# Performance work log

Measured on AMD Instinct MI355X. Metric: run time of the kernel, lower is better.

Reference implementation:

```python
import jax, jax.numpy as jnp
import numpy as np

NUM_CAPSULE = 16
DIM_CAPSULE = 64
ROUTINGS = 3
T_EPS = 1e-7


def setup_inputs() -> dict:
    key = jax.random.key(0)
    k1, k2 = jax.random.split(key)
    x = jax.random.normal(k1, (64, 512, 768), dtype=jnp.float32)
    # xavier-normal-ish init for W: [1, input_dim_capsule, num_capsule*dim_capsule]
    fan_in, fan_out = 768, NUM_CAPSULE * DIM_CAPSULE
    std = float(np.sqrt(2.0 / (fan_in + fan_out)))
    W = jax.random.normal(k2, (1, 768, NUM_CAPSULE * DIM_CAPSULE), dtype=jnp.float32) * std
    return {"x": x, "W": W}


def _squash(v, eps=T_EPS):
    # NOTE: this module's 'squash' is pure L2 normalization with eps, not the
    # classic (s^2/(1+s^2)) squash.
    s2 = jnp.sum(v * v, axis=-1, keepdims=True)
    return v / jnp.sqrt(s2 + eps)


def reference(x, W):
    B, In, _ = x.shape
    # u_hat: [B, In, num*dim] -> [B, num, In, dim]
    u = jnp.matmul(x, W).reshape(B, In, NUM_CAPSULE, DIM_CAPSULE).transpose(0, 2, 1, 3)
    b = jnp.zeros((B, NUM_CAPSULE, In), dtype=u.dtype)  # routing logits
    outputs = None
    for i in range(ROUTINGS):
        # torch code softmaxes over the num_capsule axis (after permute dance)
        c = jax.nn.softmax(b, axis=1)  # [B, num, In]
        outputs = _squash(jnp.einsum('bij,bijk->bik', c, u))  # [B, num, dim]
        if i < ROUTINGS - 1:
            b = jnp.einsum('bik,bijk->bij', outputs, u)  # [B, num, In]
    return outputs
```

## Files before the change

kernel.cpp:

```cpp
#include <hip/hip_runtime.h>
#include <hip/hip_bf16.h>
#include <stdint.h>

#define BATCH 64
#define IN_CAPS 512
#define NCAP 16
#define DCAP 64
#define GN (NCAP * DCAP)
#define GM (BATCH * IN_CAPS)
#define GK 768

typedef __bf16 bf16;
typedef __attribute__((ext_vector_type(8))) __bf16 bf16x8;
typedef __attribute__((ext_vector_type(4))) float f32x4;

__device__ inline void async16(const bf16* g, bf16* l) {
    __builtin_amdgcn_global_load_lds(
        (__attribute__((address_space(1))) void*)g,
        (__attribute__((address_space(3))) void*)l, 16, 0, 0);
}

__global__ __launch_bounds__(256) void k_convX2(const float* __restrict__ X,
                                                bf16* __restrict__ Xb,
                                                float* __restrict__ XS) {
    __shared__ float ls[GK];
    const int tid = threadIdx.x;
    ls[tid] = 0.f; ls[tid + 256] = 0.f; ls[tid + 512] = 0.f;
    __syncthreads();
    const size_t base = (size_t)blockIdx.x * (32 * GK);
    float acc[3][8] = {};
#pragma unroll
    for (int r = 0; r < 12; ++r) {
        const int off = r * 2048 + tid * 8;
        const f32x4 a0 = *(const f32x4*)(X + base + off);
        const f32x4 a1 = *(const f32x4*)(X + base + off + 4);
        bf16x8 o;
        o[0] = (bf16)a0[0]; o[1] = (bf16)a0[1]; o[2] = (bf16)a0[2]; o[3] = (bf16)a0[3];
        o[4] = (bf16)a1[0]; o[5] = (bf16)a1[1]; o[6] = (bf16)a1[2]; o[7] = (bf16)a1[3];
        *(bf16x8*)(Xb + base + off) = o;
        const int g = r % 3;
        acc[g][0] += a0[0]; acc[g][1] += a0[1];
        acc[g][2] += a0[2]; acc[g][3] += a0[3];
        acc[g][4] += a1[0]; acc[g][5] += a1[1];
        acc[g][6] += a1[2]; acc[g][7] += a1[3];
    }
    if (XS != nullptr) {
#pragma unroll
        for (int g = 0; g < 3; ++g) {
            const int cg = (g == 1) ? 512 : (g == 2) ? 256 : 0;
            const int kb = (tid * 8 + cg) % GK;
#pragma unroll
            for (int j = 0; j < 8; ++j) atomicAdd(&ls[kb + j], acc[g][j]);
        }
        __syncthreads();
        const int bidx = blockIdx.x >> 4;
        atomicAdd(&XS[(size_t)bidx * GK + tid],       ls[tid]);
        atomicAdd(&XS[(size_t)bidx * GK + tid + 256], ls[tid + 256]);
        atomicAdd(&XS[(size_t)bidx * GK + tid + 512], ls[tid + 512]);
    }
}

__global__ void k_transW(const float* __restrict__ W, bf16* __restrict__ Wt,
                         float* __restrict__ XS) {
    __shared__ bf16 t[32][33];
    const int k0 = blockIdx.x * 32;
    const int n0 = blockIdx.y * 32;
    const int tx = threadIdx.x, ty = threadIdx.y;
    if (XS != nullptr) {
        const int gid = (blockIdx.y * gridDim.x + blockIdx.x) * 256 + ty * 32 + tx;
        if (gid < BATCH * GK) XS[gid] = 0.f;
    }
#pragma unroll
    for (int r = 0; r < 4; ++r)
        t[ty + r * 8][tx] = (bf16)W[(size_t)(k0 + ty + r * 8) * GN + n0 + tx];
    __syncthreads();
#pragma unroll
    for (int r = 0; r < 4; ++r)
        Wt[(size_t)(n0 + ty + r * 8) * GK + k0 + tx] = t[tx][ty + r * 8];
}

__global__ __launch_bounds__(256) void k_out1(const float* __restrict__ XS,
                                              const float* __restrict__ W,
                                              float* __restrict__ O1) {
    __shared__ float xs[4][GK];
    __shared__ float red[4][4][64];
    const int cap = blockIdx.x & 15;
    const int bg = blockIdx.x >> 4;
    const int tid = threadIdx.x;
    const int k = tid & 63, kq = tid >> 6;
#pragma unroll
    for (int bb = 0; bb < 4; ++bb) {
        const size_t b = (size_t)(bg * 4 + bb);
        xs[bb][tid]       = XS[b * GK + tid];
        xs[bb][tid + 256] = XS[b * GK + tid + 256];
        xs[bb][tid + 512] = XS[b * GK + tid + 512];
    }
    __syncthreads();
    float acc4[4] = {0.f, 0.f, 0.f, 0.f};
    const float* wp = W + (size_t)(kq * 192) * GN + cap * 64 + k;
#pragma unroll 4
    for (int kk = 0; kk < 192; ++kk) {
        const float w = wp[(size_t)kk * GN];
        const int kx = kq * 192 + kk;
        acc4[0] += xs[0][kx] * w;
        acc4[1] += xs[1][kx] * w;
        acc4[2] += xs[2][kx] * w;
        acc4[3] += xs[3][kx] * w;
    }
#pragma unroll
    for (int bb = 0; bb < 4; ++bb) red[bb][kq][k] = acc4[bb];
    __syncthreads();
    if (tid < 64) {
#pragma unroll
        for (int bb = 0; bb < 4; ++bb) {
            float s = (red[bb][0][tid] + red[bb][1][tid] +
                       red[bb][2][tid] + red[bb][3][tid]) * 0.0625f;
            float ss = s * s;
#pragma unroll
            for (int off = 32; off >= 1; off >>= 1) ss += __shfl_xor(ss, off);
            O1[((size_t)(bg * 4 + bb) * NCAP + cap) * DCAP + tid] =
                s * rsqrtf(ss + 1e-7f);
        }
    }
}

__global__ __launch_bounds__(256) void k_gemm_async(const bf16* __restrict__ Xb,
                                                    const bf16* __restrict__ Wt,
                                                    const float* __restrict__ O1,
                                                    bf16* __restrict__ U,
                                                    float* __restrict__ BL) {
    __shared__ bf16 sA[128 * 32];
    __shared__ bf16 sB[128 * 32];

    const int tid = threadIdx.x;
    const int lane = tid & 63;
    const int wave = tid >> 6;
    const int wm = wave >> 1, wn = wave & 1;
    const int bid = blockIdx.x;
    const int swz = (bid & 7) * 256 + (bid >> 3);
    const int m0 = (swz >> 3) * 128;
    const int n0 = (swz & 7) * 128;

    const int c0 = wave * 2, c1 = wave * 2 + 1;
    const int rl = lane >> 2, cl = (lane & 3) * 8;
    const bf16* gA0 = Xb + (size_t)(m0 + c0 * 16 + rl) * GK + cl;
    const bf16* gA1 = Xb + (size_t)(m0 + c1 * 16 + rl) * GK + cl;
    const bf16* gB0 = Wt + (size_t)(n0 + c0 * 16 + rl) * GK + cl;
    const bf16* gB1 = Wt + (size_t)(n0 + c1 * 16 + rl) * GK + cl;
    bf16* lA0 = sA + c0 * 512;
    bf16* lA1 = sA + c1 * 512;
    bf16* lB0 = sB + c0 * 512;
    bf16* lB1 = sB + c1 * 512;

    f32x4 acc[4][4] = {};
    const int fr = lane & 15;
    const int fq = lane >> 4;

    for (int kt = 0; kt < GK / 32; ++kt) {
        __syncthreads();
        async16(gA0, lA0);
        async16(gA1, lA1);
        async16(gB0, lB0);
        async16(gB1, lB1);
        gA0 += 32; gA1 += 32; gB0 += 32; gB1 += 32;
        __syncthreads();

        bf16x8 af[4], bfr[4];
#pragma unroll
        for (int mi = 0; mi < 4; ++mi)
            af[mi] = *(const bf16x8*)(sA + (wm * 64 + mi * 16 + fr) * 32 + fq * 8);
#pragma unroll
        for (int ni = 0; ni < 4; ++ni)
            bfr[ni] = *(const bf16x8*)(sB + (wn * 64 + ni * 16 + fr) * 32 + fq * 8);
#pragma unroll
        for (int mi = 0; mi < 4; ++mi)
#pragma unroll
            for (int ni = 0; ni < 4; ++ni)
                acc[mi][ni] = __builtin_amdgcn_mfma_f32_16x16x32_bf16(
                    af[mi], bfr[ni], acc[mi][ni], 0, 0, 0);
    }

#pragma unroll
    for (int mi = 0; mi < 4; ++mi) {
#pragma unroll
        for (int ni = 0; ni < 4; ++ni) {
#pragma unroll
            for (int r = 0; r < 4; ++r) {
                const int m = m0 + wm * 64 + mi * 16 + fq * 4 + r;
                const int n = n0 + wn * 64 + ni * 16 + fr;
                const int bb = m >> 9, j = m & 511;
                const int ci = n >> 6, k = n & 63;
                U[(((size_t)(bb * NCAP + ci)) * IN_CAPS + j) * DCAP + k] =
                    (bf16)acc[mi][ni][r];
            }
        }
    }

    if (O1 != nullptr) {
        const int b = m0 >> 9;
        const int cap = (n0 >> 6) + wn;
        float o1v[4];
#pragma unroll
        for (int ni = 0; ni < 4; ++ni)
            o1v[ni] = O1[(size_t)b * GN + n0 + wn * 64 + ni * 16 + fr];
#pragma unroll
        for (int mi = 0; mi < 4; ++mi) {
#pragma unroll
            for (int r = 0; r < 4; ++r) {
                float p = o1v[0] * acc[mi][0][r] + o1v[1] * acc[mi][1][r] +
                          o1v[2] * acc[mi][2][r] + o1v[3] * acc[mi][3][r];
                p += __shfl_xor(p, 1);
                p += __shfl_xor(p, 2);
                p += __shfl_xor(p, 4);
                p += __shfl_xor(p, 8);
                if (fr == 0) {
                    const int j = (m0 & 511) + wm * 64 + mi * 16 + fq * 4 + r;
                    BL[((size_t)(b * NCAP + cap)) * IN_CAPS + j] = p;
                }
            }
        }
    }
}

__global__ __launch_bounds__(256) void k_gemm_inline(const float* __restrict__ X,
                                                     const bf16* __restrict__ Wt,
                                                     bf16* __restrict__ U) {
    __shared__ bf16 sA[128 * 32];
    __shared__ bf16 sB[128 * 32];
    const int tid = threadIdx.x;
    const int lane = tid & 63;
    const int wave = tid >> 6;
    const int wm = wave >> 1, wn = wave & 1;
    const int m0 = blockIdx.x * 128;
    const int n0 = blockIdx.y * 128;
    const int srow = tid >> 2;
    const int scol = (tid & 3) * 8;
    f32x4 acc[4][4] = {};
    const int fr = lane & 15;
    const int fq = lane >> 4;
    for (int kt = 0; kt < GK / 32; ++kt) {
        const int kb = kt * 32;
        bf16x8 a0, a1, b0, b1;
        {
            const float* p = X + (size_t)(m0 + srow) * GK + kb + scol;
            const f32x4 x0 = *(const f32x4*)p, x1 = *(const f32x4*)(p + 4);
            const float* q = X + (size_t)(m0 + srow + 64) * GK + kb + scol;
            const f32x4 y0 = *(const f32x4*)q, y1 = *(const f32x4*)(q + 4);
#pragma unroll
            for (int c = 0; c < 4; ++c) {
                a0[c] = (bf16)x0[c]; a0[c + 4] = (bf16)x1[c];
                a1[c] = (bf16)y0[c]; a1[c + 4] = (bf16)y1[c];
            }
        }
        b0 = *(const bf16x8*)(Wt + (size_t)(n0 + srow) * GK + kb + scol);
        b1 = *(const bf16x8*)(Wt + (size_t)(n0 + srow + 64) * GK + kb + scol);
        __syncthreads();
        *(bf16x8*)(sA + srow * 32 + scol) = a0;
        *(bf16x8*)(sA + (srow + 64) * 32 + scol) = a1;
        *(bf16x8*)(sB + srow * 32 + scol) = b0;
        *(bf16x8*)(sB + (srow + 64) * 32 + scol) = b1;
        __syncthreads();
        bf16x8 af[4], bfr[4];
#pragma unroll
        for (int mi = 0; mi < 4; ++mi)
            af[mi] = *(const bf16x8*)(sA + (wm * 64 + mi * 16 + fr) * 32 + fq * 8);
#pragma unroll
        for (int ni = 0; ni < 4; ++ni)
            bfr[ni] = *(const bf16x8*)(sB + (wn * 64 + ni * 16 + fr) * 32 + fq * 8);
#pragma unroll
        for (int mi = 0; mi < 4; ++mi)
#pragma unroll
            for (int ni = 0; ni < 4; ++ni)
                acc[mi][ni] = __builtin_amdgcn_mfma_f32_16x16x32_bf16(
                    af[mi], bfr[ni], acc[mi][ni], 0, 0, 0);
    }
#pragma unroll
    for (int mi = 0; mi < 4; ++mi) {
#pragma unroll
        for (int ni = 0; ni < 4; ++ni) {
#pragma unroll
            for (int r = 0; r < 4; ++r) {
                const int m = m0 + wm * 64 + mi * 16 + fq * 4 + r;
                const int n = n0 + wn * 64 + ni * 16 + fr;
                const int bb = m >> 9, j = m & 511;
                const int ci = n >> 6, k = n & 63;
                U[(((size_t)(bb * NCAP + ci)) * IN_CAPS + j) * DCAP + k] =
                    (bf16)acc[mi][ni][r];
            }
        }
    }
}

__global__ __launch_bounds__(256) void k_route(const bf16* __restrict__ U,
                                               const float* __restrict__ BLin,
                                               float* __restrict__ BLout,
                                               float* __restrict__ OutC,
                                               int mode) {
    __shared__ float sc[IN_CAPS];
    __shared__ float red2[4][64];
    __shared__ float sout[64];
    const int bi = blockIdx.x;
    const int b = bi >> 4, cap = bi & 15;
    const int tid = threadIdx.x;
    const int lane = tid & 63;
    const int wave = tid >> 6;
    const size_t ubase = (size_t)bi * IN_CAPS * DCAP;

    if (mode == 0) {
        sc[tid] = 0.0625f;
        sc[tid + 256] = 0.0625f;
    } else {
#pragma unroll
        for (int h = 0; h < 2; ++h) {
            const int j = tid + h * 256;
            const float* p = BLin + (size_t)b * NCAP * IN_CAPS + j;
            float v[16], mx = -1e30f;
#pragma unroll
            for (int i = 0; i < 16; ++i) {
                v[i] = p[(size_t)i * IN_CAPS];
                mx = fmaxf(mx, v[i]);
            }
            float s = 0.f;
#pragma unroll
            for (int i = 0; i < 16; ++i) s += __expf(v[i] - mx);
            sc[j] = __expf(v[cap] - mx) / s;
        }
    }
    __syncthreads();

    const int g = tid & 7;
    const int jr = tid >> 3;

    float acc[8] = {};
#pragma unroll
    for (int it = 0; it < 16; ++it) {
        const int j = it * 32 + jr;
        const bf16x8 v = *(const bf16x8*)(U + ubase + (size_t)it * 2048 + tid * 8);
        const float cv = sc[j];
#pragma unroll
        for (int c = 0; c < 8; ++c) acc[c] += cv * (float)v[c];
    }
#pragma unroll
    for (int c = 0; c < 8; ++c) {
        acc[c] += __shfl_xor(acc[c], 8);
        acc[c] += __shfl_xor(acc[c], 16);
        acc[c] += __shfl_xor(acc[c], 32);
    }
    if ((lane >> 3) == 0) {
#pragma unroll
        for (int c = 0; c < 8; ++c) red2[wave][lane * 8 + c] = acc[c];
    }
    __syncthreads();

    if (tid < 64) {
        float s = red2[0][tid] + red2[1][tid] + red2[2][tid] + red2[3][tid];
        float ss = s * s;
#pragma unroll
        for (int off = 32; off >= 1; off >>= 1) ss += __shfl_xor(ss, off);
        const float val = s * rsqrtf(ss + 1e-7f);
        sout[tid] = val;
        if (mode == 2) OutC[(size_t)bi * DCAP + tid] = val;
    }
    if (mode == 2) return;
    __syncthreads();

    const f32x4 o0 = *(const f32x4*)(sout + g * 8);
    const f32x4 o1 = *(const f32x4*)(sout + g * 8 + 4);
#pragma unroll
    for (int it = 0; it < 16; ++it) {
        const int j = it * 32 + jr;
        const bf16x8 v = *(const bf16x8*)(U + ubase + (size_t)it * 2048 + tid * 8);
        float p = o0[0] * (float)v[0] + o0[1] * (float)v[1] +
                  o0[2] * (float)v[2] + o0[3] * (float)v[3] +
                  o1[0] * (float)v[4] + o1[1] * (float)v[5] +
                  o1[2] * (float)v[6] + o1[3] * (float)v[7];
        p += __shfl_xor(p, 1);
        p += __shfl_xor(p, 2);
        p += __shfl_xor(p, 4);
        if (g == 0) BLout[((size_t)(b * NCAP + cap)) * IN_CAPS + j] = p;
    }
}

extern "C" void kernel_launch(void* const* d_in, const int* in_sizes, int n_in,
                              void* d_out, int out_size, void* d_ws, size_t ws_size,
                              hipStream_t stream) {
    const float* X = (const float*)d_in[0];
    const float* W = (const float*)d_in[1];
    float* OutC = (float*)d_out;

    const size_t u_bytes = (size_t)BATCH * NCAP * IN_CAPS * DCAP * sizeof(bf16);
    const size_t xb_bytes = (size_t)GM * GK * sizeof(bf16);
    const size_t wt_bytes = (size_t)GN * GK * sizeof(bf16);
    const size_t bl_bytes = (size_t)BATCH * NCAP * IN_CAPS * sizeof(float);
    const size_t xs_bytes = (size_t)BATCH * GK * sizeof(float);
    const size_t o1_bytes = (size_t)BATCH * GN * sizeof(float);
    char* ws = (char*)d_ws;

    const size_t need_full = u_bytes + xb_bytes + wt_bytes + bl_bytes + xs_bytes + o1_bytes;
    const size_t need_async = u_bytes + xb_bytes + wt_bytes + bl_bytes;
    const size_t need_small = u_bytes + wt_bytes + bl_bytes;

    bf16* U = (bf16*)ws;

    if (ws_size >= need_full) {
        bf16* Xb = (bf16*)(ws + u_bytes);
        bf16* Wt = (bf16*)(ws + u_bytes + xb_bytes);
        float* BL = (float*)(ws + u_bytes + xb_bytes + wt_bytes);
        float* XS = (float*)(ws + u_bytes + xb_bytes + wt_bytes + bl_bytes);
        float* O1 = (float*)(ws + u_bytes + xb_bytes + wt_bytes + bl_bytes + xs_bytes);
        float* BLtmp = (float*)Xb;

        k_transW<<<dim3(GK / 32, GN / 32), dim3(32, 8), 0, stream>>>(W, Wt, XS);
        k_convX2<<<GM / 32, 256, 0, stream>>>(X, Xb, XS);
        k_out1<<<256, 256, 0, stream>>>(XS, W, O1);
        k_gemm_async<<<2048, 256, 0, stream>>>(Xb, Wt, O1, U, BL);
        k_route<<<BATCH * NCAP, 256, 0, stream>>>(U, BL, BLtmp, OutC, 1);
        k_route<<<BATCH * NCAP, 256, 0, stream>>>(U, BLtmp, nullptr, OutC, 2);
    } else if (ws_size >= need_async) {
        bf16* Xb = (bf16*)(ws + u_bytes);
        bf16* Wt = (bf16*)(ws + u_bytes + xb_bytes);
        float* BL = (float*)(ws + u_bytes + xb_bytes + wt_bytes);
        float* BLtmp = (float*)Xb;
        k_transW<<<dim3(GK / 32, GN / 32), dim3(32, 8), 0, stream>>>(W, Wt, nullptr);
        k_convX2<<<GM / 32, 256, 0, stream>>>(X, Xb, nullptr);
        k_gemm_async<<<2048, 256, 0, stream>>>(Xb, Wt, nullptr, U, BL);
        k_route<<<BATCH * NCAP, 256, 0, stream>>>(U, nullptr, BL, OutC, 0);
        k_route<<<BATCH * NCAP, 256, 0, stream>>>(U, BL, BLtmp, OutC, 1);
        k_route<<<BATCH * NCAP, 256, 0, stream>>>(U, BLtmp, nullptr, OutC, 2);
    } else if (ws_size >= need_small) {
        bf16* Wt = (bf16*)(ws + u_bytes);
        float* BL = (float*)(ws + u_bytes + wt_bytes);
        k_transW<<<dim3(GK / 32, GN / 32), dim3(32, 8), 0, stream>>>(W, Wt, nullptr);
        k_gemm_inline<<<dim3(GM / 128, GN / 128), 256, 0, stream>>>(X, Wt, U);
        k_route<<<BATCH * NCAP, 256, 0, stream>>>(U, BL, BL, OutC, 0);
        k_route<<<BATCH * NCAP, 256, 0, stream>>>(U, BL, BL, OutC, 1);
        k_route<<<BATCH * NCAP, 256, 0, stream>>>(U, BL, BL, OutC, 2);
    }
}
```

Baseline: 287.5 us.

## Reassociate routing to avoid materializing u_hat, working in input-feature space

Replaces the full x·W GEMM that produced the large u_hat tensor with an algebraic reformulation. Routing logits are computed as x·(W·o), with Z = W_cap·o per batch and capsule. Capsule outputs come from W^T applied to the softmax-weighted sum of x rows. This removes the 1024-wide GEMM and the write and re-read of u_hat, replacing them with small GEMVs, a narrow MFMA kernel for the logits, and a partial-sum reduction over Yp. The cost is more kernel launches, an extra Yp workspace, and bf16 rounding of Z and x at different points than before, which may shift numerics.

After: 331.4 us. 1.15x slower.

```diff
diff --git a/kernel.cpp b/kernel.cpp
--- a/kernel.cpp
+++ b/kernel.cpp
@@ -14,11 +14,6 @@
 typedef __attribute__((ext_vector_type(8))) __bf16 bf16x8;
 typedef __attribute__((ext_vector_type(4))) float f32x4;
 
-__device__ inline void async16(const bf16* g, bf16* l) {
-    __builtin_amdgcn_global_load_lds(
-        (__attribute__((address_space(1))) void*)g,
-        (__attribute__((address_space(3))) void*)l, 16, 0, 0);
-}
 
 __global__ __launch_bounds__(256) void k_convX2(const float* __restrict__ X,
                                                 bf16* __restrict__ Xb,
@@ -79,11 +74,13 @@
         Wt[(size_t)(n0 + ty + r * 8) * GK + k0 + tx] = t[tx][ty + r * 8];
 }
 
-__global__ __launch_bounds__(256) void k_out1(const float* __restrict__ XS,
-                                              const float* __restrict__ W,
-                                              float* __restrict__ O1) {
+__global__ __launch_bounds__(256) void k_out1z(const float* __restrict__ XS,
+                                               const float* __restrict__ W,
+                                               const bf16* __restrict__ Wt,
+                                               float* __restrict__ Z) {
     __shared__ float xs[4][GK];
     __shared__ float red[4][4][64];
+    __shared__ float sout4[4][64];
     const int cap = blockIdx.x & 15;
     const int bg = blockIdx.x >> 4;
     const int tid = threadIdx.x;
@@ -118,107 +115,165 @@
             float ss = s * s;
 #pragma unroll
             for (int off = 32; off >= 1; off >>= 1) ss += __shfl_xor(ss, off);
-            O1[((size_t)(bg * 4 + bb) * NCAP + cap) * DCAP + tid] =
-                s * rsqrtf(ss + 1e-7f);
-        }
-    }
-}
-
-__global__ __launch_bounds__(256) void k_gemm_async(const bf16* __restrict__ Xb,
-                                                    const bf16* __restrict__ Wt,
-                                                    const float* __restrict__ O1,
-                                                    bf16* __restrict__ U,
-                                                    float* __restrict__ BL) {
-    __shared__ bf16 sA[128 * 32];
-    __shared__ bf16 sB[128 * 32];
-
+            sout4[bb][tid] = s * rsqrtf(ss + 1e-7f);
+        }
+    }
+    __syncthreads();
+#pragma unroll
+    for (int bb = 0; bb < 4; ++bb) {
+        const size_t bi = (size_t)(bg * 4 + bb) * NCAP + cap;
+#pragma unroll
+        for (int r = 0; r < 3; ++r) {
+            const int kk = r * 256 + tid;
+            float z = 0.f;
+#pragma unroll 8
+            for (int d = 0; d < 64; ++d)
+                z += (float)Wt[(size_t)(cap * 64 + d) * GK + kk] * sout4[bb][d];
+            Z[bi * GK + kk] = z;
+        }
+    }
+}
+
+__global__ __launch_bounds__(256) void k_bl(const float* __restrict__ Z,
+                                            const bf16* __restrict__ Xb,
+                                            float* __restrict__ BLo) {
+    __shared__ __align__(16) bf16 za[16 * 776];
+    const int b  = blockIdx.x >> 2;
+    const int js = blockIdx.x & 3;
     const int tid = threadIdx.x;
     const int lane = tid & 63;
     const int wave = tid >> 6;
-    const int wm = wave >> 1, wn = wave & 1;
-    const int bid = blockIdx.x;
-    const int swz = (bid & 7) * 256 + (bid >> 3);
-    const int m0 = (swz >> 3) * 128;
-    const int n0 = (swz & 7) * 128;
-
-    const int c0 = wave * 2, c1 = wave * 2 + 1;
-    const int rl = lane >> 2, cl = (lane & 3) * 8;
-    const bf16* gA0 = Xb + (size_t)(m0 + c0 * 16 + rl) * GK + cl;
-    const bf16* gA1 = Xb + (size_t)(m0 + c1 * 16 + rl) * GK + cl;
-    const bf16* gB0 = Wt + (size_t)(n0 + c0 * 16 + rl) * GK + cl;
-    const bf16* gB1 = Wt + (size_t)(n0 + c1 * 16 + rl) * GK + cl;
-    bf16* lA0 = sA + c0 * 512;
-    bf16* lA1 = sA + c1 * 512;
-    bf16* lB0 = sB + c0 * 512;
-    bf16* lB1 = sB + c1 * 512;
-
-    f32x4 acc[4][4] = {};
-    const int fr = lane & 15;
-    const int fq = lane >> 4;
-
+    const int fr = lane & 15, fq = lane >> 4;
+
+#pragma unroll
+    for (int cap = 0; cap < 16; ++cap) {
+        const float* zp = Z + ((size_t)b * NCAP + cap) * GK;
+#pragma unroll
+        for (int r = 0; r < 3; ++r) {
+            const int kk = r * 256 + tid;
+            za[cap * 776 + kk] = (bf16)zp[kk];
+        }
+    }
+    __syncthreads();
+
+    const int j0 = js * 128 + wave * 32;
+    f32x4 acc[2] = {};
     for (int kt = 0; kt < GK / 32; ++kt) {
-        __syncthreads();
-        async16(gA0, lA0);
-        async16(gA1, lA1);
-        async16(gB0, lB0);
-        async16(gB1, lB1);
-        gA0 += 32; gA1 += 32; gB0 += 32; gB1 += 32;
-        __syncthreads();
-
-        bf16x8 af[4], bfr[4];
-#pragma unroll
-        for (int mi = 0; mi < 4; ++mi)
-            af[mi] = *(const bf16x8*)(sA + (wm * 64 + mi * 16 + fr) * 32 + fq * 8);
-#pragma unroll
-        for (int ni = 0; ni < 4; ++ni)
-            bfr[ni] = *(const bf16x8*)(sB + (wn * 64 + ni * 16 + fr) * 32 + fq * 8);
-#pragma unroll
-        for (int mi = 0; mi < 4; ++mi)
-#pragma unroll
-            for (int ni = 0; ni < 4; ++ni)
-                acc[mi][ni] = __builtin_amdgcn_mfma_f32_16x16x32_bf16(
-                    af[mi], bfr[ni], acc[mi][ni], 0, 0, 0);
-    }
-
-#pragma unroll
-    for (int mi = 0; mi < 4; ++mi) {
-#pragma unroll
-        for (int ni = 0; ni < 4; ++ni) {
-#pragma unroll
-            for (int r = 0; r < 4; ++r) {
-                const int m = m0 + wm * 64 + mi * 16 + fq * 4 + r;
-                const int n = n0 + wn * 64 + ni * 16 + fr;
-                const int bb = m >> 9, j = m & 511;
-                const int ci = n >> 6, k = n & 63;
-                U[(((size_t)(bb * NCAP + ci)) * IN_CAPS + j) * DCAP + k] =
-                    (bf16)acc[mi][ni][r];
-            }
-        }
-    }
-
-    if (O1 != nullptr) {
-        const int b = m0 >> 9;
-        const int cap = (n0 >> 6) + wn;
-        float o1v[4];
-#pragma unroll
-        for (int ni = 0; ni < 4; ++ni)
-            o1v[ni] = O1[(size_t)b * GN + n0 + wn * 64 + ni * 16 + fr];
-#pragma unroll
-        for (int mi = 0; mi < 4; ++mi) {
-#pragma unroll
-            for (int r = 0; r < 4; ++r) {
-                float p = o1v[0] * acc[mi][0][r] + o1v[1] * acc[mi][1][r] +
-                          o1v[2] * acc[mi][2][r] + o1v[3] * acc[mi][3][r];
-                p += __shfl_xor(p, 1);
-                p += __shfl_xor(p, 2);
-                p += __shfl_xor(p, 4);
-                p += __shfl_xor(p, 8);
-                if (fr == 0) {
-                    const int j = (m0 & 511) + wm * 64 + mi * 16 + fq * 4 + r;
-                    BL[((size_t)(b * NCAP + cap)) * IN_CAPS + j] = p;
-                }
-            }
-        }
+        const bf16x8 af = *(const bf16x8*)(za + fr * 776 + kt * 32 + fq * 8);
+#pragma unroll
+        for (int ni = 0; ni < 2; ++ni) {
+            const bf16x8 bf = *(const bf16x8*)(
+                Xb + ((size_t)b * IN_CAPS + j0 + ni * 16 + fr) * GK + kt * 32 + fq * 8);
+            acc[ni] = __builtin_amdgcn_mfma_f32_16x16x32_bf16(af, bf, acc[ni], 0, 0, 0);
+        }
+    }
+#pragma unroll
+    for (int ni = 0; ni < 2; ++ni)
+#pragma unroll
+        for (int r = 0; r < 4; ++r) {
+            const int cap = fq * 4 + r;
+            const int j = j0 + ni * 16 + fr;
+            BLo[((size_t)b * NCAP + cap) * IN_CAPS + j] = acc[ni][r];
+        }
+}
+
+__global__ __launch_bounds__(256) void k_y(const float* __restrict__ BLi,
+                                           const bf16* __restrict__ Xb,
+                                           float* __restrict__ Yp) {
+    __shared__ __align__(16) float sc[64][16];
+    const int b  = blockIdx.x >> 3;
+    const int js = blockIdx.x & 7;
+    const int tid = threadIdx.x;
+    if (tid < 64) {
+        const int j = js * 64 + tid;
+        const float* p = BLi + (size_t)b * NCAP * IN_CAPS + j;
+        float v[16], mx = -1e30f;
+#pragma unroll
+        for (int i = 0; i < 16; ++i) { v[i] = p[(size_t)i * IN_CAPS]; mx = fmaxf(mx, v[i]); }
+        float s = 0.f;
+#pragma unroll
+        for (int i = 0; i < 16; ++i) { v[i] = __expf(v[i] - mx); s += v[i]; }
+        const float inv = 1.f / s;
+#pragma unroll
+        for (int i = 0; i < 16; ++i) sc[tid][i] = v[i] * inv;
+    }
+    __syncthreads();
+
+    float acc[16][3] = {};
+    for (int jl = 0; jl < 64; ++jl) {
+        const bf16* xp = Xb + ((size_t)b * IN_CAPS + js * 64 + jl) * GK + tid;
+        const float x0 = (float)xp[0];
+        const float x1 = (float)xp[256];
+        const float x2 = (float)xp[512];
+        const f32x4 c0 = *(const f32x4*)(&sc[jl][0]);
+        const f32x4 c1 = *(const f32x4*)(&sc[jl][4]);
+        const f32x4 c2 = *(const f32x4*)(&sc[jl][8]);
+        const f32x4 c3 = *(const f32x4*)(&sc[jl][12]);
+#pragma unroll
+        for (int i = 0; i < 4; ++i) {
+            acc[i][0]      += c0[i] * x0; acc[i][1]      += c0[i] * x1; acc[i][2]      += c0[i] * x2;
+            acc[4 + i][0]  += c1[i] * x0; acc[4 + i][1]  += c1[i] * x1; acc[4 + i][2]  += c1[i] * x2;
+            acc[8 + i][0]  += c2[i] * x0; acc[8 + i][1]  += c2[i] * x1; acc[8 + i][2]  += c2[i] * x2;
+            acc[12 + i][0] += c3[i] * x0; acc[12 + i][1] += c3[i] * x1; acc[12 + i][2] += c3[i] * x2;
+        }
+    }
+#pragma unroll
+    for (int cap = 0; cap < 16; ++cap) {
+        float* yp = Yp + ((size_t)blockIdx.x * NCAP + cap) * GK;
+        yp[tid] = acc[cap][0]; yp[tid + 256] = acc[cap][1]; yp[tid + 512] = acc[cap][2];
+    }
+}
+
+__global__ __launch_bounds__(256) void k_oz(const float* __restrict__ Yp,
+                                            const float* __restrict__ W,
+                                            const bf16* __restrict__ Wt,
+                                            float* __restrict__ Zo,
+                                            float* __restrict__ OutC) {
+    __shared__ float ly[GK];
+    __shared__ float red[4][64];
+    __shared__ float sout[64];
+    const int bi = blockIdx.x;
+    const int b = bi >> 4, cap = bi & 15;
+    const int tid = threadIdx.x;
+#pragma unroll
+    for (int r = 0; r < 3; ++r) {
+        const int kk = r * 256 + tid;
+        float s = 0.f;
+#pragma unroll
+        for (int js = 0; js < 8; ++js)
+            s += Yp[(((size_t)b * 8 + js) * NCAP + cap) * GK + kk];
+        ly[kk] = s;
+    }
+    __syncthreads();
+    const int d = tid & 63, kq = tid >> 6;
+    {
+        float a = 0.f;
+        const float* wp = W + (size_t)(kq * 192) * GN + cap * 64 + d;
+#pragma unroll 4
+        for (int kk = 0; kk < 192; ++kk)
+            a += ly[kq * 192 + kk] * wp[(size_t)kk * GN];
+        red[kq][d] = a;
+    }
+    __syncthreads();
+    if (tid < 64) {
+        float s = red[0][tid] + red[1][tid] + red[2][tid] + red[3][tid];
+        float ss = s * s;
+#pragma unroll
+        for (int off = 32; off >= 1; off >>= 1) ss += __shfl_xor(ss, off);
+        const float val = s * rsqrtf(ss + 1e-7f);
+        sout[tid] = val;
+        if (OutC != nullptr) OutC[(size_t)bi * DCAP + tid] = val;
+    }
+    if (OutC != nullptr) return;
+    __syncthreads();
+#pragma unroll
+    for (int r = 0; r < 3; ++r) {
+        const int kk = r * 256 + tid;
+        float z = 0.f;
+#pragma unroll 8
+        for (int dd = 0; dd < 64; ++dd)
+            z += (float)Wt[(size_t)(cap * 64 + dd) * GK + kk] * sout[dd];
+        Zo[(size_t)bi * GK + kk] = z;
     }
 }
 
@@ -388,46 +443,38 @@
     const float* W = (const float*)d_in[1];
     float* OutC = (float*)d_out;
 
-    const size_t u_bytes = (size_t)BATCH * NCAP * IN_CAPS * DCAP * sizeof(bf16);
     const size_t xb_bytes = (size_t)GM * GK * sizeof(bf16);
     const size_t wt_bytes = (size_t)GN * GK * sizeof(bf16);
+    const size_t xs_bytes = (size_t)BATCH * GK * sizeof(float);
+    const size_t z_bytes  = (size_t)BATCH * NCAP * GK * sizeof(float);
     const size_t bl_bytes = (size_t)BATCH * NCAP * IN_CAPS * sizeof(float);
-    const size_t xs_bytes = (size_t)BATCH * GK * sizeof(float);
-    const size_t o1_bytes = (size_t)BATCH * GN * sizeof(float);
+    const size_t yp_bytes = (size_t)BATCH * 8 * NCAP * GK * sizeof(float);
     char* ws = (char*)d_ws;
 
-    const size_t need_full = u_bytes + xb_bytes + wt_bytes + bl_bytes + xs_bytes + o1_bytes;
-    const size_t need_async = u_bytes + xb_bytes + wt_bytes + bl_bytes;
-    const size_t need_small = u_bytes + wt_bytes + bl_bytes;
-
-    bf16* U = (bf16*)ws;
-
-    if (ws_size >= need_full) {
-        bf16* Xb = (bf16*)(ws + u_bytes);
-        bf16* Wt = (bf16*)(ws + u_bytes + xb_bytes);
-        float* BL = (float*)(ws + u_bytes + xb_bytes + wt_bytes);
-        float* XS = (float*)(ws + u_bytes + xb_bytes + wt_bytes + bl_bytes);
-        float* O1 = (float*)(ws + u_bytes + xb_bytes + wt_bytes + bl_bytes + xs_bytes);
-        float* BLtmp = (float*)Xb;
+    const size_t need_new = xb_bytes + wt_bytes + xs_bytes + z_bytes + bl_bytes + yp_bytes;
+
+    const size_t u_bytes = (size_t)BATCH * NCAP * IN_CAPS * DCAP * sizeof(bf16);
+    const size_t need_old = u_bytes + wt_bytes + bl_bytes;
+
+    if (ws_size >= need_new) {
+        bf16* Xb  = (bf16*)ws;
+        bf16* Wt  = (bf16*)(ws + xb_bytes);
+        float* XS = (float*)(ws + xb_bytes + wt_bytes);
+        float* Z  = (float*)(ws + xb_bytes + wt_bytes + xs_bytes);
+        float* BL = (float*)(ws + xb_bytes + wt_bytes + xs_bytes + z_bytes);
+        float* Yp = (float*)(ws + xb_bytes + wt_bytes + xs_bytes + z_bytes + bl_bytes);
 
         k_transW<<<dim3(GK / 32, GN / 32), dim3(32, 8), 0, stream>>>(W, Wt, XS);
         k_convX2<<<GM / 32, 256, 0, stream>>>(X, Xb, XS);
-        k_out1<<<256, 256, 0, stream>>>(XS, W, O1);
-        k_gemm_async<<<2048, 256, 0, stream>>>(Xb, Wt, O1, U, BL);
-        k_route<<<BATCH * NCAP, 256, 0, stream>>>(U, BL, BLtmp, OutC, 1);
-        k_route<<<BATCH * NCAP, 256, 0, stream>>>(U, BLtmp, nullptr, OutC, 2);
-    } else if (ws_size >= need_async) {
-        bf16* Xb = (bf16*)(ws + u_bytes);
-        bf16* Wt = (bf16*)(ws + u_bytes + xb_bytes);
-        float* BL = (float*)(ws + u_bytes + xb_bytes + wt_bytes);
-        float* BLtmp = (float*)Xb;
-        k_transW<<<dim3(GK / 32, GN / 32), dim3(32, 8), 0, stream>>>(W, Wt, nullptr);
-        k_convX2<<<GM / 32, 256, 0, stream>>>(X, Xb, nullptr);
-        k_gemm_async<<<2048, 256, 0, stream>>>(Xb, Wt, nullptr, U, BL);
-        k_route<<<BATCH * NCAP, 256, 0, stream>>>(U, nullptr, BL, OutC, 0);
-        k_route<<<BATCH * NCAP, 256, 0, stream>>>(U, BL, BLtmp, OutC, 1);
-        k_route<<<BATCH * NCAP, 256, 0, stream>>>(U, BLtmp, nullptr, OutC, 2);
-    } else if (ws_size >= need_small) {
+        k_out1z<<<256, 256, 0, stream>>>(XS, W, Wt, Z);
+        k_bl<<<BATCH * 4, 256, 0, stream>>>(Z, Xb, BL);
+        k_y<<<BATCH * 8, 256, 0, stream>>>(BL, Xb, Yp);
+        k_oz<<<BATCH * NCAP, 256, 0, stream>>>(Yp, W, Wt, Z, nullptr);
+        k_bl<<<BATCH * 4, 256, 0, stream>>>(Z, Xb, BL);
+        k_y<<<BATCH * 8, 256, 0, stream>>>(BL, Xb, Yp);
+        k_oz<<<BATCH * NCAP, 256, 0, stream>>>(Yp, W, Wt, nullptr, OutC);
+    } else if (ws_size >= need_old) {
+        bf16* U = (bf16*)ws;
         bf16* Wt = (bf16*)(ws + u_bytes);
         float* BL = (float*)(ws + u_bytes + wt_bytes);
         k_transW<<<dim3(GK / 32, GN / 32), dim3(32, 8), 0, stream>>>(W, Wt, nullptr);
```
